# Kernel optimization log

Measured on AMD Instinct MI355X. Metric: run time of the kernel, lower is better.

Reference implementation:

```python
import jax, jax.numpy as jnp
import numpy as np

NSIDE_SEND, NSIDE_REC = 128, 64
NPIX_SEND = 12 * NSIDE_SEND * NSIDE_SEND  # 196608 edges (one per fine pixel)
NPIX_REC = 12 * NSIDE_REC * NSIDE_REC     # 49152 coarse pixels
RATIO = NPIX_SEND // NPIX_REC             # 4 children per coarse pixel
B, F_IN = 2, 128
EMBED_OUT, LIN_OUT = 64, 128
LIN_IN = EMBED_OUT + F_IN


def setup_inputs() -> dict:
    key = jax.random.key(0)
    ks = jax.random.split(key, 9)
    s = 0.02
    # buffers (deterministic, from HEALPix nested ordering)
    edge_attr = (jnp.arange(NPIX_SEND, dtype=jnp.float32) % RATIO).reshape(-1, 1)
    edge_rec = (jnp.arange(NPIX_SEND, dtype=jnp.int32) // RATIO)
    return {
        "x": jax.random.normal(ks[0], (B, NPIX_SEND, F_IN), dtype=jnp.float32),
        "edge_attr": edge_attr,
        "edge_rec": edge_rec,
        # edge embedder MLP: 1 -> 64 -> 64
        "we1": jax.random.normal(ks[1], (1, EMBED_OUT), dtype=jnp.float32) * s,
        "be1": jnp.zeros((EMBED_OUT,), dtype=jnp.float32),
        "we2": jax.random.normal(ks[2], (EMBED_OUT, EMBED_OUT), dtype=jnp.float32) * s,
        "be2": jnp.zeros((EMBED_OUT,), dtype=jnp.float32),
        # final FeedForward: 192 -> 128 -> 128
        "wf1": jax.random.normal(ks[3], (LIN_IN, LIN_OUT), dtype=jnp.float32) * s,
        "bf1": jnp.zeros((LIN_OUT,), dtype=jnp.float32),
        "wf2": jax.random.normal(ks[4], (LIN_OUT, LIN_OUT), dtype=jnp.float32) * s,
        "bf2": jnp.zeros((LIN_OUT,), dtype=jnp.float32),
    }


def reference(x, edge_attr, edge_rec, we1, be1, we2, be2, wf1, bf1, wf2, bf2):
    # edge embedding MLP over the per-edge scalar attribute  [E, embed_out]
    e = jax.nn.gelu(edge_attr @ we1 + be1) @ we2 + be2
    # broadcast over batch and concat with node features  [B, E, lin_in]
    vm = jnp.concatenate([jnp.broadcast_to(e[None], (x.shape[0],) + e.shape), x], axis=-1)
    # scatter_sum over receiver pixels along the edge axis  [B, R, lin_in]
    agg = jax.vmap(lambda v: jax.ops.segment_sum(v, edge_rec, num_segments=NPIX_REC))(vm)
    # final FeedForward
    return jax.nn.gelu(agg @ wf1 + bf1) @ wf2 + bf2
```

## Files before the change

kernel.cpp:

```cpp
#include <hip/hip_runtime.h>


#define NPIX_SEND 196608
#define NPIX_REC  49152
#define F_IN      128
#define EMB       64
#define LIN_OUT   128
#define MTOT      98304
#define BM        64
#define NBLOCKS   (MTOT / BM)

#define WS_C1 0
#define WS_W1 512
#define WS_W2 (512 + 32768)

#define LDS_H 0
#define LDS_W 16384
#define LDS_BYTES 49152

typedef __attribute__((ext_vector_type(4))) float f32x4;
typedef __attribute__((ext_vector_type(8))) short bf16x8;

__device__ __forceinline__ float gelu_tanh(float v) {
  float u = 0.7978845608028654f * (v + 0.044715f * v * v * v);
  float e = __expf(2.0f * u);
  return 0.5f * v * (1.0f + (1.0f - 2.0f / (e + 1.0f)));
}

__device__ __forceinline__ unsigned short f2bf(float f) {
  unsigned int u = __builtin_bit_cast(unsigned int, f);
  u += 0x7FFFu + ((u >> 16) & 1u);
  return (unsigned short)(u >> 16);
}

__global__ void heal_prep(const float* __restrict__ we1, const float* __restrict__ be1,
                          const float* __restrict__ we2, const float* __restrict__ be2,
                          const float* __restrict__ wf1, const float* __restrict__ bf1,
                          const float* __restrict__ wf2,
                          unsigned char* __restrict__ ws) {
  int t = threadIdx.x;
  if (blockIdx.x == 0) {
    __shared__ float G[EMB];
    __shared__ float esum[EMB];
    if (t < EMB) {
      float w = we1[t], b = be1[t];
      float g = 0.f;
      #pragma unroll
      for (int a = 0; a < 4; ++a) g += gelu_tanh((float)a * w + b);
      G[t] = g;
    }
    __syncthreads();
    if (t < EMB) {
      float s = 4.0f * be2[t];
      for (int h = 0; h < EMB; ++h) s += G[h] * we2[h * EMB + t];
      esum[t] = s;
    }
    __syncthreads();
    if (t < LIN_OUT) {
      float s = bf1[t];
      for (int i = 0; i < EMB; ++i) s += esum[i] * wf1[i * LIN_OUT + t];
      ((float*)(ws + WS_C1))[t] = s;
    }
  } else {
    int e0 = (blockIdx.x - 1) * 512 + t * 2;
    #pragma unroll
    for (int u = 0; u < 2; ++u) {
      int e = e0 + u;
      int idx = e & 16383;
      int n = idx >> 7;
      int k = idx & 127;
      float v;
      unsigned int base;
      if (e < 16384) { v = wf1[(EMB + k) * LIN_OUT + n]; base = WS_W1; }
      else           { v = wf2[k * LIN_OUT + n];         base = WS_W2; }
      unsigned int byte = (unsigned int)(n * 256 + k * 2) ^ (unsigned int)((n & 7) << 4);
      *(unsigned short*)(ws + base + byte) = f2bf(v);
    }
  }
}

__global__ __launch_bounds__(256, 3) void heal_main(
    const float* __restrict__ x, const float* __restrict__ bf2,
    const unsigned char* __restrict__ ws, float* __restrict__ out) {
  extern __shared__ unsigned char smem[];
  const int t = threadIdx.x;

  {
    const uint4* src = (const uint4*)(ws + WS_W1);
    uint4* dst = (uint4*)(smem + LDS_W);
    #pragma unroll
    for (int i = 0; i < 8; ++i) dst[t + 256 * i] = src[t + 256 * i];
  }
  uint4 w2reg[8];
  {
    const uint4* src2 = (const uint4*)(ws + WS_W2);
    #pragma unroll
    for (int i = 0; i < 8; ++i) w2reg[i] = src2[t + 256 * i];
  }

  const int gr0 = blockIdx.x * BM;
  const int b   = gr0 / NPIX_REC;
  const int rr0 = gr0 - b * NPIX_REC;
  const float* xb = x + (size_t)(b * NPIX_SEND + 4 * rr0) * F_IN;
  {
    const int kq = t & 31;
    const int mg = t >> 5;
    #pragma unroll
    for (int it = 0; it < 8; ++it) {
      int m = mg + it * 8;
      const f32x4* rp = (const f32x4*)(xb + (size_t)(4 * m) * F_IN) + kq;
      f32x4 s = rp[0] + rp[32] + rp[64] + rp[96];
      unsigned int lo = (unsigned int)f2bf(s.x) | ((unsigned int)f2bf(s.y) << 16);
      unsigned int hi = (unsigned int)f2bf(s.z) | ((unsigned int)f2bf(s.w) << 16);
      unsigned int byte = (unsigned int)(m * 256 + kq * 8) ^ (unsigned int)((m & 7) << 4);
      uint2 val; val.x = lo; val.y = hi;
      *(uint2*)(smem + LDS_H + byte) = val;
    }
  }

  const int w  = t >> 6;
  const int l  = t & 63;
  const int cr = l & 15;
  const int kg = l >> 4;
  float c1v[8], b2v[8];
  {
    const float* c1 = (const float*)(ws + WS_C1);
    #pragma unroll
    for (int f = 0; f < 8; ++f) { c1v[f] = c1[f * 16 + cr]; b2v[f] = bf2[f * 16 + cr]; }
  }

  __syncthreads();

  const int arow = w * 16 + cr;
  const unsigned int aswz = (unsigned int)((arow & 7) << 4);
  const unsigned int abase = (unsigned int)(arow * 256 + kg * 16);
  const unsigned int bswz = (unsigned int)((cr & 7) << 4);

  bf16x8 a[4];
  #pragma unroll
  for (int kk = 0; kk < 4; ++kk)
    a[kk] = *(const bf16x8*)(smem + LDS_H + ((abase + kk * 64) ^ aswz));

  f32x4 acc[8];
  #pragma unroll
  for (int f = 0; f < 8; ++f) {
    f32x4 z = {0.f, 0.f, 0.f, 0.f};
    acc[f] = z;
    unsigned int nbase = (unsigned int)((f * 16 + cr) * 256 + kg * 16);
    #pragma unroll
    for (int kk = 0; kk < 4; ++kk) {
      bf16x8 bfrag = *(const bf16x8*)(smem + LDS_W + ((nbase + kk * 64) ^ bswz));
      acc[f] = __builtin_amdgcn_mfma_f32_16x16x32_bf16(a[kk], bfrag, acc[f], 0, 0, 0);
    }
  }

  #pragma unroll
  for (int f = 0; f < 8; ++f) {
    #pragma unroll
    for (int q = 0; q < 4; ++q) {
      float v = gelu_tanh(acc[f][q] + c1v[f]);
      int hrow = w * 16 + kg * 4 + q;
      unsigned int byte = (unsigned int)(hrow * 256 + (f * 16 + cr) * 2)
                        ^ (unsigned int)((hrow & 7) << 4);
      *(unsigned short*)(smem + LDS_H + byte) = f2bf(v);
    }
  }

  __syncthreads();

  bf16x8 a2[4];
  #pragma unroll
  for (int kk = 0; kk < 4; ++kk)
    a2[kk] = *(const bf16x8*)(smem + LDS_H + ((abase + kk * 64) ^ aswz));

  {
    uint4* dst = (uint4*)(smem + LDS_W);
    #pragma unroll
    for (int i = 0; i < 8; ++i) dst[t + 256 * i] = w2reg[i];
  }
  __syncthreads();

  f32x4 acc2[8];
  #pragma unroll
  for (int f = 0; f < 8; ++f) {
    f32x4 z = {0.f, 0.f, 0.f, 0.f};
    acc2[f] = z;
    unsigned int nbase = (unsigned int)((f * 16 + cr) * 256 + kg * 16);
    #pragma unroll
    for (int kk = 0; kk < 4; ++kk) {
      bf16x8 bfrag = *(const bf16x8*)(smem + LDS_W + ((nbase + kk * 64) ^ bswz));
      acc2[f] = __builtin_amdgcn_mfma_f32_16x16x32_bf16(a2[kk], bfrag, acc2[f], 0, 0, 0);
    }
  }

  #pragma unroll
  for (int q = 0; q < 4; ++q) {
    int orow = gr0 + w * 16 + kg * 4 + q;
    float* op = out + (size_t)orow * LIN_OUT;
    #pragma unroll
    for (int f = 0; f < 8; ++f)
      op[f * 16 + cr] = acc2[f][q] + b2v[f];
  }
}

extern "C" void kernel_launch(void* const* d_in, const int* in_sizes, int n_in,
                              void* d_out, int out_size, void* d_ws, size_t ws_size,
                              hipStream_t stream) {
  const float* x   = (const float*)d_in[0];
  const float* we1 = (const float*)d_in[3];
  const float* be1 = (const float*)d_in[4];
  const float* we2 = (const float*)d_in[5];
  const float* be2 = (const float*)d_in[6];
  const float* wf1 = (const float*)d_in[7];
  const float* bf1 = (const float*)d_in[8];
  const float* wf2 = (const float*)d_in[9];
  const float* bf2 = (const float*)d_in[10];
  float* out = (float*)d_out;
  unsigned char* ws = (unsigned char*)d_ws;

  hipLaunchKernelGGL(heal_prep, dim3(65), dim3(256), 0, stream,
                     we1, be1, we2, be2, wf1, bf1, wf2, ws);
  hipLaunchKernelGGL(heal_main, dim3(NBLOCKS), dim3(256), LDS_BYTES, stream,
                     x, bf2, ws, out);
}
```

Measured before the change: 70.45 us.

## Stream weights in half-tiles through smaller LDS to raise occupancy

Splits each 128x128 weight matrix into two 64-column halves staged one at a time through a 16 KB LDS buffer, cutting LDS from 48 KB to 32 KB and register-held weights from 8 to 4 uint4 per thread, with launch bounds raised to 4 blocks per CU. Each wave now gathers its own 16 rows of x, and the x reads use nontemporal loads. The aim is more resident blocks to hide the memory-bound x reads. In exchange it adds several extra __syncthreads and LDS refills per block.

```diff
diff --git a/kernel.cpp b/kernel.cpp
--- a/kernel.cpp
+++ b/kernel.cpp
@@ -14,9 +14,9 @@
 #define WS_W1 512
 #define WS_W2 (512 + 32768)
 
-#define LDS_H 0
-#define LDS_W 16384
-#define LDS_BYTES 49152
+#define LDS_X 0
+#define LDS_B 16384
+#define LDS_BYTES 32768
 
 typedef __attribute__((ext_vector_type(4))) float f32x4;
 typedef __attribute__((ext_vector_type(8))) short bf16x8;
@@ -79,56 +79,49 @@
   }
 }
 
-__global__ __launch_bounds__(256, 3) void heal_main(
+__global__ __launch_bounds__(256, 4) void heal_main(
     const float* __restrict__ x, const float* __restrict__ bf2,
     const unsigned char* __restrict__ ws, float* __restrict__ out) {
   extern __shared__ unsigned char smem[];
   const int t = threadIdx.x;
-
-  {
-    const uint4* src = (const uint4*)(ws + WS_W1);
-    uint4* dst = (uint4*)(smem + LDS_W);
-    #pragma unroll
-    for (int i = 0; i < 8; ++i) dst[t + 256 * i] = src[t + 256 * i];
-  }
-  uint4 w2reg[8];
-  {
-    const uint4* src2 = (const uint4*)(ws + WS_W2);
-    #pragma unroll
-    for (int i = 0; i < 8; ++i) w2reg[i] = src2[t + 256 * i];
-  }
+  const int w = t >> 6, l = t & 63;
+  const int cr = l & 15, kg = l >> 4;
 
   const int gr0 = blockIdx.x * BM;
   const int b   = gr0 / NPIX_REC;
   const int rr0 = gr0 - b * NPIX_REC;
   const float* xb = x + (size_t)(b * NPIX_SEND + 4 * rr0) * F_IN;
-  {
-    const int kq = t & 31;
-    const int mg = t >> 5;
+
+  uint4 wregA[4], wregB[4];
+
+  {
+    const uint4* src = (const uint4*)(ws + WS_W1);
+    #pragma unroll
+    for (int i = 0; i < 4; ++i) wregA[i] = src[t + 256 * i];
+  }
+  {
+    const int kq = l & 31;
+    const int rh = l >> 5;
     #pragma unroll
     for (int it = 0; it < 8; ++it) {
-      int m = mg + it * 8;
+      int m = w * 16 + it * 2 + rh;
       const f32x4* rp = (const f32x4*)(xb + (size_t)(4 * m) * F_IN) + kq;
-      f32x4 s = rp[0] + rp[32] + rp[64] + rp[96];
+      f32x4 s = __builtin_nontemporal_load(rp)
+              + __builtin_nontemporal_load(rp + 32)
+              + __builtin_nontemporal_load(rp + 64)
+              + __builtin_nontemporal_load(rp + 96);
       unsigned int lo = (unsigned int)f2bf(s.x) | ((unsigned int)f2bf(s.y) << 16);
       unsigned int hi = (unsigned int)f2bf(s.z) | ((unsigned int)f2bf(s.w) << 16);
       unsigned int byte = (unsigned int)(m * 256 + kq * 8) ^ (unsigned int)((m & 7) << 4);
       uint2 val; val.x = lo; val.y = hi;
-      *(uint2*)(smem + LDS_H + byte) = val;
-    }
-  }
-
-  const int w  = t >> 6;
-  const int l  = t & 63;
-  const int cr = l & 15;
-  const int kg = l >> 4;
-  float c1v[8], b2v[8];
-  {
-    const float* c1 = (const float*)(ws + WS_C1);
-    #pragma unroll
-    for (int f = 0; f < 8; ++f) { c1v[f] = c1[f * 16 + cr]; b2v[f] = bf2[f * 16 + cr]; }
-  }
-
+      *(uint2*)(smem + LDS_X + byte) = val;
+    }
+  }
+  {
+    uint4* dst = (uint4*)(smem + LDS_B);
+    #pragma unroll
+    for (int i = 0; i < 4; ++i) dst[t + 256 * i] = wregA[i];
+  }
   __syncthreads();
 
   const int arow = w * 16 + cr;
@@ -139,67 +132,145 @@
   bf16x8 a[4];
   #pragma unroll
   for (int kk = 0; kk < 4; ++kk)
-    a[kk] = *(const bf16x8*)(smem + LDS_H + ((abase + kk * 64) ^ aswz));
-
-  f32x4 acc[8];
-  #pragma unroll
-  for (int f = 0; f < 8; ++f) {
-    f32x4 z = {0.f, 0.f, 0.f, 0.f};
-    acc[f] = z;
-    unsigned int nbase = (unsigned int)((f * 16 + cr) * 256 + kg * 16);
-    #pragma unroll
-    for (int kk = 0; kk < 4; ++kk) {
-      bf16x8 bfrag = *(const bf16x8*)(smem + LDS_W + ((nbase + kk * 64) ^ bswz));
-      acc[f] = __builtin_amdgcn_mfma_f32_16x16x32_bf16(a[kk], bfrag, acc[f], 0, 0, 0);
-    }
-  }
-
-  #pragma unroll
-  for (int f = 0; f < 8; ++f) {
+    a[kk] = *(const bf16x8*)(smem + LDS_X + ((abase + kk * 64) ^ aswz));
+  {
+    const uint4* src = (const uint4*)(ws + WS_W1 + 16384);
+    #pragma unroll
+    for (int i = 0; i < 4; ++i) wregB[i] = src[t + 256 * i];
+  }
+  f32x4 acc0[4], acc1[4];
+  #pragma unroll
+  for (int f = 0; f < 4; ++f) {
+    f32x4 z = {0.f, 0.f, 0.f, 0.f};
+    acc0[f] = z;
+    unsigned int nbase = (unsigned int)((f * 16 + cr) * 256 + kg * 16);
+    #pragma unroll
+    for (int kk = 0; kk < 4; ++kk) {
+      bf16x8 bfrag = *(const bf16x8*)(smem + LDS_B + ((nbase + kk * 64) ^ bswz));
+      acc0[f] = __builtin_amdgcn_mfma_f32_16x16x32_bf16(a[kk], bfrag, acc0[f], 0, 0, 0);
+    }
+  }
+  __syncthreads();
+
+  {
+    uint4* dst = (uint4*)(smem + LDS_B);
+    #pragma unroll
+    for (int i = 0; i < 4; ++i) dst[t + 256 * i] = wregB[i];
+  }
+  {
+    const uint4* src = (const uint4*)(ws + WS_W2);
+    #pragma unroll
+    for (int i = 0; i < 4; ++i) wregA[i] = src[t + 256 * i];
+  }
+  {
+    const float* c1 = (const float*)(ws + WS_C1);
+    #pragma unroll
+    for (int f = 0; f < 4; ++f) {
+      float c1v = c1[f * 16 + cr];
+      #pragma unroll
+      for (int q = 0; q < 4; ++q) {
+        float v = gelu_tanh(acc0[f][q] + c1v);
+        int hrow = w * 16 + kg * 4 + q;
+        unsigned int byte = (unsigned int)(hrow * 256 + (f * 16 + cr) * 2)
+                          ^ (unsigned int)((hrow & 7) << 4);
+        *(unsigned short*)(smem + LDS_X + byte) = f2bf(v);
+      }
+    }
+  }
+  __syncthreads();
+
+  #pragma unroll
+  for (int f = 0; f < 4; ++f) {
+    f32x4 z = {0.f, 0.f, 0.f, 0.f};
+    acc1[f] = z;
+    unsigned int nbase = (unsigned int)((f * 16 + cr) * 256 + kg * 16);
+    #pragma unroll
+    for (int kk = 0; kk < 4; ++kk) {
+      bf16x8 bfrag = *(const bf16x8*)(smem + LDS_B + ((nbase + kk * 64) ^ bswz));
+      acc1[f] = __builtin_amdgcn_mfma_f32_16x16x32_bf16(a[kk], bfrag, acc1[f], 0, 0, 0);
+    }
+  }
+  __syncthreads();
+
+  {
+    uint4* dst = (uint4*)(smem + LDS_B);
+    #pragma unroll
+    for (int i = 0; i < 4; ++i) dst[t + 256 * i] = wregA[i];
+  }
+  {
+    const uint4* src = (const uint4*)(ws + WS_W2 + 16384);
+    #pragma unroll
+    for (int i = 0; i < 4; ++i) wregB[i] = src[t + 256 * i];
+  }
+  {
+    const float* c1 = (const float*)(ws + WS_C1);
+    #pragma unroll
+    for (int f = 0; f < 4; ++f) {
+      float c1v = c1[64 + f * 16 + cr];
+      #pragma unroll
+      for (int q = 0; q < 4; ++q) {
+        float v = gelu_tanh(acc1[f][q] + c1v);
+        int hrow = w * 16 + kg * 4 + q;
+        unsigned int byte = (unsigned int)(hrow * 256 + (64 + f * 16 + cr) * 2)
+                          ^ (unsigned int)((hrow & 7) << 4);
+        *(unsigned short*)(smem + LDS_X + byte) = f2bf(v);
+      }
+    }
+  }
+  __syncthreads();
+
+  bf16x8 a2[4];
+  #pragma unroll
+  for (int kk = 0; kk < 4; ++kk)
+    a2[kk] = *(const bf16x8*)(smem + LDS_X + ((abase + kk * 64) ^ aswz));
+  #pragma unroll
+  for (int f = 0; f < 4; ++f) {
+    f32x4 z = {0.f, 0.f, 0.f, 0.f};
+    acc0[f] = z;
+    unsigned int nbase = (unsigned int)((f * 16 + cr) * 256 + kg * 16);
+    #pragma unroll
+    for (int kk = 0; kk < 4; ++kk) {
+      bf16x8 bfrag = *(const bf16x8*)(smem + LDS_B + ((nbase + kk * 64) ^ bswz));
+      acc0[f] = __builtin_amdgcn_mfma_f32_16x16x32_bf16(a2[kk], bfrag, acc0[f], 0, 0, 0);
+    }
+  }
+  #pragma unroll
+  for (int f = 0; f < 4; ++f) {
+    float b2 = bf2[f * 16 + cr];
     #pragma unroll
     for (int q = 0; q < 4; ++q) {
-      float v = gelu_tanh(acc[f][q] + c1v[f]);
-      int hrow = w * 16 + kg * 4 + q;
-      unsigned int byte = (unsigned int)(hrow * 256 + (f * 16 + cr) * 2)
-                        ^ (unsigned int)((hrow & 7) << 4);
-      *(unsigned short*)(smem + LDS_H + byte) = f2bf(v);
-    }
-  }
-
-  __syncthreads();
-
-  bf16x8 a2[4];
-  #pragma unroll
-  for (int kk = 0; kk < 4; ++kk)
-    a2[kk] = *(const bf16x8*)(smem + LDS_H + ((abase + kk * 64) ^ aswz));
-
-  {
-    uint4* dst = (uint4*)(smem + LDS_W);
-    #pragma unroll
-    for (int i = 0; i < 8; ++i) dst[t + 256 * i] = w2reg[i];
-  }
-  __syncthreads();
-
-  f32x4 acc2[8];
-  #pragma unroll
-  for (int f = 0; f < 8; ++f) {
-    f32x4 z = {0.f, 0.f, 0.f, 0.f};
-    acc2[f] = z;
-    unsigned int nbase = (unsigned int)((f * 16 + cr) * 256 + kg * 16);
-    #pragma unroll
-    for (int kk = 0; kk < 4; ++kk) {
-      bf16x8 bfrag = *(const bf16x8*)(smem + LDS_W + ((nbase + kk * 64) ^ bswz));
-      acc2[f] = __builtin_amdgcn_mfma_f32_16x16x32_bf16(a2[kk], bfrag, acc2[f], 0, 0, 0);
-    }
-  }
-
-  #pragma unroll
-  for (int q = 0; q < 4; ++q) {
-    int orow = gr0 + w * 16 + kg * 4 + q;
-    float* op = out + (size_t)orow * LIN_OUT;
-    #pragma unroll
-    for (int f = 0; f < 8; ++f)
-      op[f * 16 + cr] = acc2[f][q] + b2v[f];
+      int orow = gr0 + w * 16 + kg * 4 + q;
+      out[(size_t)orow * LIN_OUT + f * 16 + cr] = acc0[f][q] + b2;
+    }
+  }
+  __syncthreads();
+
+  {
+    uint4* dst = (uint4*)(smem + LDS_B);
+    #pragma unroll
+    for (int i = 0; i < 4; ++i) dst[t + 256 * i] = wregB[i];
+  }
+  __syncthreads();
+
+  #pragma unroll
+  for (int f = 0; f < 4; ++f) {
+    f32x4 z = {0.f, 0.f, 0.f, 0.f};
+    acc1[f] = z;
+    unsigned int nbase = (unsigned int)((f * 16 + cr) * 256 + kg * 16);
+    #pragma unroll
+    for (int kk = 0; kk < 4; ++kk) {
+      bf16x8 bfrag = *(const bf16x8*)(smem + LDS_B + ((nbase + kk * 64) ^ bswz));
+      acc1[f] = __builtin_amdgcn_mfma_f32_16x16x32_bf16(a2[kk], bfrag, acc1[f], 0, 0, 0);
+    }
+  }
+  #pragma unroll
+  for (int f = 0; f < 4; ++f) {
+    float b2 = bf2[64 + f * 16 + cr];
+    #pragma unroll
+    for (int q = 0; q < 4; ++q) {
+      int orow = gr0 + w * 16 + kg * 4 + q;
+      out[(size_t)orow * LIN_OUT + 64 + f * 16 + cr] = acc1[f][q] + b2;
+    }
   }
 }
 
```

New measurement: 85.09 us. +20.8%, slower.

## Read MFMA weight fragments from global/L2 and drop block barriers

Applied to the files above, without the earlier changes.

The weight matrices are no longer staged in LDS. Each wave now loads its B fragments directly from the workspace in global memory, which should stay hot in L2 and L1. This removes the per-block weight copy, the register-held W2, and all __syncthreads, because each wave only touches its own 16 rows of the hidden tile in LDS. LDS shrinks from 48KB to 16KB and launch bounds go from 3 to 4 blocks per CU. The cost is repeated global or cache loads of weights by every wave.

```diff
diff --git a/kernel.cpp b/kernel.cpp
--- a/kernel.cpp
+++ b/kernel.cpp
@@ -13,10 +13,6 @@
 #define WS_C1 0
 #define WS_W1 512
 #define WS_W2 (512 + 32768)
-
-#define LDS_H 0
-#define LDS_W 16384
-#define LDS_BYTES 49152
 
 typedef __attribute__((ext_vector_type(4))) float f32x4;
 typedef __attribute__((ext_vector_type(8))) short bf16x8;
@@ -73,133 +69,114 @@
       unsigned int base;
       if (e < 16384) { v = wf1[(EMB + k) * LIN_OUT + n]; base = WS_W1; }
       else           { v = wf2[k * LIN_OUT + n];         base = WS_W2; }
-      unsigned int byte = (unsigned int)(n * 256 + k * 2) ^ (unsigned int)((n & 7) << 4);
-      *(unsigned short*)(ws + base + byte) = f2bf(v);
-    }
-  }
-}
-
-__global__ __launch_bounds__(256, 3) void heal_main(
+      *(unsigned short*)(ws + base + (unsigned int)(n * 256 + k * 2)) = f2bf(v);
+    }
+  }
+}
+
+__global__ __launch_bounds__(256, 4) void heal_main(
     const float* __restrict__ x, const float* __restrict__ bf2,
     const unsigned char* __restrict__ ws, float* __restrict__ out) {
-  extern __shared__ unsigned char smem[];
+  __shared__ unsigned char smem[16384];
   const int t = threadIdx.x;
-
-  {
-    const uint4* src = (const uint4*)(ws + WS_W1);
-    uint4* dst = (uint4*)(smem + LDS_W);
-    #pragma unroll
-    for (int i = 0; i < 8; ++i) dst[t + 256 * i] = src[t + 256 * i];
-  }
-  uint4 w2reg[8];
-  {
-    const uint4* src2 = (const uint4*)(ws + WS_W2);
-    #pragma unroll
-    for (int i = 0; i < 8; ++i) w2reg[i] = src2[t + 256 * i];
-  }
+  const int w = t >> 6, l = t & 63;
+  const int cr = l & 15, kg = l >> 4;
 
   const int gr0 = blockIdx.x * BM;
   const int b   = gr0 / NPIX_REC;
   const int rr0 = gr0 - b * NPIX_REC;
   const float* xb = x + (size_t)(b * NPIX_SEND + 4 * rr0) * F_IN;
+
   {
-    const int kq = t & 31;
-    const int mg = t >> 5;
-    #pragma unroll
+    const int kq = l & 31;
+    const int rh = l >> 5;
+    #pragma unroll 2
     for (int it = 0; it < 8; ++it) {
-      int m = mg + it * 8;
+      int m = w * 16 + it * 2 + rh;
       const f32x4* rp = (const f32x4*)(xb + (size_t)(4 * m) * F_IN) + kq;
       f32x4 s = rp[0] + rp[32] + rp[64] + rp[96];
       unsigned int lo = (unsigned int)f2bf(s.x) | ((unsigned int)f2bf(s.y) << 16);
       unsigned int hi = (unsigned int)f2bf(s.z) | ((unsigned int)f2bf(s.w) << 16);
       unsigned int byte = (unsigned int)(m * 256 + kq * 8) ^ (unsigned int)((m & 7) << 4);
       uint2 val; val.x = lo; val.y = hi;
-      *(uint2*)(smem + LDS_H + byte) = val;
-    }
-  }
-
-  const int w  = t >> 6;
-  const int l  = t & 63;
-  const int cr = l & 15;
-  const int kg = l >> 4;
-  float c1v[8], b2v[8];
-  {
-    const float* c1 = (const float*)(ws + WS_C1);
-    #pragma unroll
-    for (int f = 0; f < 8; ++f) { c1v[f] = c1[f * 16 + cr]; b2v[f] = bf2[f * 16 + cr]; }
-  }
-
-  __syncthreads();
+      *(uint2*)(smem + byte) = val;
+    }
+  }
 
   const int arow = w * 16 + cr;
   const unsigned int aswz = (unsigned int)((arow & 7) << 4);
   const unsigned int abase = (unsigned int)(arow * 256 + kg * 16);
-  const unsigned int bswz = (unsigned int)((cr & 7) << 4);
 
   bf16x8 a[4];
   #pragma unroll
   for (int kk = 0; kk < 4; ++kk)
-    a[kk] = *(const bf16x8*)(smem + LDS_H + ((abase + kk * 64) ^ aswz));
-
-  f32x4 acc[8];
-  #pragma unroll
-  for (int f = 0; f < 8; ++f) {
-    f32x4 z = {0.f, 0.f, 0.f, 0.f};
-    acc[f] = z;
-    unsigned int nbase = (unsigned int)((f * 16 + cr) * 256 + kg * 16);
-    #pragma unroll
-    for (int kk = 0; kk < 4; ++kk) {
-      bf16x8 bfrag = *(const bf16x8*)(smem + LDS_W + ((nbase + kk * 64) ^ bswz));
-      acc[f] = __builtin_amdgcn_mfma_f32_16x16x32_bf16(a[kk], bfrag, acc[f], 0, 0, 0);
-    }
-  }
-
-  #pragma unroll
-  for (int f = 0; f < 8; ++f) {
+    a[kk] = *(const bf16x8*)(smem + ((abase + kk * 64) ^ aswz));
+
+  const float* c1 = (const float*)(ws + WS_C1);
+  const unsigned char* wg1 = ws + WS_W1;
+  const unsigned char* wg2 = ws + WS_W2;
+
+  #pragma unroll
+  for (int fp = 0; fp < 4; ++fp) {
+    const int f0 = fp * 2, f1 = f0 + 1;
+    const unsigned int n0 = (unsigned int)((f0 * 16 + cr) * 256 + kg * 16);
+    const unsigned int n1 = (unsigned int)((f1 * 16 + cr) * 256 + kg * 16);
+    bf16x8 b0[4], b1[4];
+    #pragma unroll
+    for (int kk = 0; kk < 4; ++kk) {
+      b0[kk] = *(const bf16x8*)(wg1 + n0 + kk * 64);
+      b1[kk] = *(const bf16x8*)(wg1 + n1 + kk * 64);
+    }
+    f32x4 acc0 = {0.f, 0.f, 0.f, 0.f}, acc1 = {0.f, 0.f, 0.f, 0.f};
+    #pragma unroll
+    for (int kk = 0; kk < 4; ++kk) {
+      acc0 = __builtin_amdgcn_mfma_f32_16x16x32_bf16(a[kk], b0[kk], acc0, 0, 0, 0);
+      acc1 = __builtin_amdgcn_mfma_f32_16x16x32_bf16(a[kk], b1[kk], acc1, 0, 0, 0);
+    }
+    float c10 = c1[f0 * 16 + cr], c11 = c1[f1 * 16 + cr];
     #pragma unroll
     for (int q = 0; q < 4; ++q) {
-      float v = gelu_tanh(acc[f][q] + c1v[f]);
       int hrow = w * 16 + kg * 4 + q;
-      unsigned int byte = (unsigned int)(hrow * 256 + (f * 16 + cr) * 2)
-                        ^ (unsigned int)((hrow & 7) << 4);
-      *(unsigned short*)(smem + LDS_H + byte) = f2bf(v);
-    }
-  }
-
-  __syncthreads();
+      unsigned int hswz = (unsigned int)((hrow & 7) << 4);
+      float v0 = gelu_tanh(acc0[q] + c10);
+      float v1 = gelu_tanh(acc1[q] + c11);
+      unsigned int byte0 = ((unsigned int)(hrow * 256 + (f0 * 16 + cr) * 2)) ^ hswz;
+      unsigned int byte1 = ((unsigned int)(hrow * 256 + (f1 * 16 + cr) * 2)) ^ hswz;
+      *(unsigned short*)(smem + byte0) = f2bf(v0);
+      *(unsigned short*)(smem + byte1) = f2bf(v1);
+    }
+  }
 
   bf16x8 a2[4];
   #pragma unroll
   for (int kk = 0; kk < 4; ++kk)
-    a2[kk] = *(const bf16x8*)(smem + LDS_H + ((abase + kk * 64) ^ aswz));
-
-  {
-    uint4* dst = (uint4*)(smem + LDS_W);
-    #pragma unroll
-    for (int i = 0; i < 8; ++i) dst[t + 256 * i] = w2reg[i];
-  }
-  __syncthreads();
-
-  f32x4 acc2[8];
-  #pragma unroll
-  for (int f = 0; f < 8; ++f) {
-    f32x4 z = {0.f, 0.f, 0.f, 0.f};
-    acc2[f] = z;
-    unsigned int nbase = (unsigned int)((f * 16 + cr) * 256 + kg * 16);
-    #pragma unroll
-    for (int kk = 0; kk < 4; ++kk) {
-      bf16x8 bfrag = *(const bf16x8*)(smem + LDS_W + ((nbase + kk * 64) ^ bswz));
-      acc2[f] = __builtin_amdgcn_mfma_f32_16x16x32_bf16(a2[kk], bfrag, acc2[f], 0, 0, 0);
-    }
-  }
-
-  #pragma unroll
-  for (int q = 0; q < 4; ++q) {
-    int orow = gr0 + w * 16 + kg * 4 + q;
-    float* op = out + (size_t)orow * LIN_OUT;
-    #pragma unroll
-    for (int f = 0; f < 8; ++f)
-      op[f * 16 + cr] = acc2[f][q] + b2v[f];
+    a2[kk] = *(const bf16x8*)(smem + ((abase + kk * 64) ^ aswz));
+
+  #pragma unroll
+  for (int fp = 0; fp < 4; ++fp) {
+    const int f0 = fp * 2, f1 = f0 + 1;
+    const unsigned int n0 = (unsigned int)((f0 * 16 + cr) * 256 + kg * 16);
+    const unsigned int n1 = (unsigned int)((f1 * 16 + cr) * 256 + kg * 16);
+    bf16x8 b0[4], b1[4];
+    #pragma unroll
+    for (int kk = 0; kk < 4; ++kk) {
+      b0[kk] = *(const bf16x8*)(wg2 + n0 + kk * 64);
+      b1[kk] = *(const bf16x8*)(wg2 + n1 + kk * 64);
+    }
+    f32x4 acc0 = {0.f, 0.f, 0.f, 0.f}, acc1 = {0.f, 0.f, 0.f, 0.f};
+    #pragma unroll
+    for (int kk = 0; kk < 4; ++kk) {
+      acc0 = __builtin_amdgcn_mfma_f32_16x16x32_bf16(a2[kk], b0[kk], acc0, 0, 0, 0);
+      acc1 = __builtin_amdgcn_mfma_f32_16x16x32_bf16(a2[kk], b1[kk], acc1, 0, 0, 0);
+    }
+    float b20 = bf2[f0 * 16 + cr], b21 = bf2[f1 * 16 + cr];
+    #pragma unroll
+    for (int q = 0; q < 4; ++q) {
+      int orow = gr0 + w * 16 + kg * 4 + q;
+      float* op = out + (size_t)orow * LIN_OUT;
+      op[f0 * 16 + cr] = acc0[q] + b20;
+      op[f1 * 16 + cr] = acc1[q] + b21;
+    }
   }
 }
 
@@ -220,6 +197,6 @@
 
   hipLaunchKernelGGL(heal_prep, dim3(65), dim3(256), 0, stream,
                      we1, be1, we2, be2, wf1, bf1, wf2, ws);
-  hipLaunchKernelGGL(heal_main, dim3(NBLOCKS), dim3(256), LDS_BYTES, stream,
+  hipLaunchKernelGGL(heal_main, dim3(NBLOCKS), dim3(256), 0, stream,
                      x, bf2, ws, out);
 }
```

Measured after the change: 74.83 us. +6.2%, slower.

## Split child-pixel summation into a separate kernel writing bf16 aggregates

Applied to the files above, without the earlier changes.

Moves the 4-way child summation of x and the bf16 conversion out of the main GEMM kernel into a dedicated streaming kernel that writes a compact bf16 buffer to workspace. The main kernel then loads pre-aggregated bf16 rows into LDS instead of reading fp32 x. The aim is to decouple the bandwidth-bound reduction from the MFMA kernel, which runs with limited occupancy. The cost is an extra launch plus writing and re-reading an intermediate buffer of about 25 MB.

```diff
diff --git a/kernel.cpp b/kernel.cpp
--- a/kernel.cpp
+++ b/kernel.cpp
@@ -13,8 +13,9 @@
 #define WS_C1 0
 #define WS_W1 512
 #define WS_W2 (512 + 32768)
-
-#define LDS_H 0
+#define WS_XS 131072
+
+#define LDS_X 0
 #define LDS_W 16384
 #define LDS_BYTES 49152
 
@@ -79,8 +80,27 @@
   }
 }
 
+__global__ void heal_xsum(const float* __restrict__ x, unsigned int* __restrict__ xs) {
+  size_t j = (size_t)blockIdx.x * 256 + threadIdx.x;
+  size_t m = j >> 4;
+  int c = (int)(j & 15);
+  const f32x4* p = (const f32x4*)(x + (m * 4) * F_IN) + c * 2;
+  f32x4 a0 = p[0],  a1 = p[1];
+  f32x4 b0 = p[32], b1 = p[33];
+  f32x4 c0 = p[64], c1 = p[65];
+  f32x4 d0 = p[96], d1 = p[97];
+  f32x4 s0 = (a0 + b0) + (c0 + d0);
+  f32x4 s1 = (a1 + b1) + (c1 + d1);
+  uint4 o;
+  o.x = (unsigned int)f2bf(s0.x) | ((unsigned int)f2bf(s0.y) << 16);
+  o.y = (unsigned int)f2bf(s0.z) | ((unsigned int)f2bf(s0.w) << 16);
+  o.z = (unsigned int)f2bf(s1.x) | ((unsigned int)f2bf(s1.y) << 16);
+  o.w = (unsigned int)f2bf(s1.z) | ((unsigned int)f2bf(s1.w) << 16);
+  *(uint4*)(xs + j * 4) = o;
+}
+
 __global__ __launch_bounds__(256, 3) void heal_main(
-    const float* __restrict__ x, const float* __restrict__ bf2,
+    const unsigned char* __restrict__ xs, const float* __restrict__ bf2,
     const unsigned char* __restrict__ ws, float* __restrict__ out) {
   extern __shared__ unsigned char smem[];
   const int t = threadIdx.x;
@@ -99,22 +119,16 @@
   }
 
   const int gr0 = blockIdx.x * BM;
-  const int b   = gr0 / NPIX_REC;
-  const int rr0 = gr0 - b * NPIX_REC;
-  const float* xb = x + (size_t)(b * NPIX_SEND + 4 * rr0) * F_IN;
-  {
-    const int kq = t & 31;
-    const int mg = t >> 5;
-    #pragma unroll
-    for (int it = 0; it < 8; ++it) {
-      int m = mg + it * 8;
-      const f32x4* rp = (const f32x4*)(xb + (size_t)(4 * m) * F_IN) + kq;
-      f32x4 s = rp[0] + rp[32] + rp[64] + rp[96];
-      unsigned int lo = (unsigned int)f2bf(s.x) | ((unsigned int)f2bf(s.y) << 16);
-      unsigned int hi = (unsigned int)f2bf(s.z) | ((unsigned int)f2bf(s.w) << 16);
-      unsigned int byte = (unsigned int)(m * 256 + kq * 8) ^ (unsigned int)((m & 7) << 4);
-      uint2 val; val.x = lo; val.y = hi;
-      *(uint2*)(smem + LDS_H + byte) = val;
+  {
+    const int kq2 = t & 15;
+    const int r0  = t >> 4;
+    const uint4* src = (const uint4*)(xs + (size_t)gr0 * 256);
+    #pragma unroll
+    for (int it = 0; it < 4; ++it) {
+      int r = r0 + it * 16;
+      uint4 v = src[r * 16 + kq2];
+      unsigned int byte = (unsigned int)(r * 256 + kq2 * 16) ^ (unsigned int)((r & 7) << 4);
+      *(uint4*)(smem + LDS_X + byte) = v;
     }
   }
 
@@ -139,7 +153,7 @@
   bf16x8 a[4];
   #pragma unroll
   for (int kk = 0; kk < 4; ++kk)
-    a[kk] = *(const bf16x8*)(smem + LDS_H + ((abase + kk * 64) ^ aswz));
+    a[kk] = *(const bf16x8*)(smem + LDS_X + ((abase + kk * 64) ^ aswz));
 
   f32x4 acc[8];
   #pragma unroll
@@ -162,7 +176,7 @@
       int hrow = w * 16 + kg * 4 + q;
       unsigned int byte = (unsigned int)(hrow * 256 + (f * 16 + cr) * 2)
                         ^ (unsigned int)((hrow & 7) << 4);
-      *(unsigned short*)(smem + LDS_H + byte) = f2bf(v);
+      *(unsigned short*)(smem + LDS_X + byte) = f2bf(v);
     }
   }
 
@@ -171,7 +185,7 @@
   bf16x8 a2[4];
   #pragma unroll
   for (int kk = 0; kk < 4; ++kk)
-    a2[kk] = *(const bf16x8*)(smem + LDS_H + ((abase + kk * 64) ^ aswz));
+    a2[kk] = *(const bf16x8*)(smem + LDS_X + ((abase + kk * 64) ^ aswz));
 
   {
     uint4* dst = (uint4*)(smem + LDS_W);
@@ -220,6 +234,8 @@
 
   hipLaunchKernelGGL(heal_prep, dim3(65), dim3(256), 0, stream,
                      we1, be1, we2, be2, wf1, bf1, wf2, ws);
+  hipLaunchKernelGGL(heal_xsum, dim3(6144), dim3(256), 0, stream,
+                     x, (unsigned int*)(ws + WS_XS));
   hipLaunchKernelGGL(heal_main, dim3(NBLOCKS), dim3(256), LDS_BYTES, stream,
-                     x, bf2, ws, out);
-}
+                     (const unsigned char*)(ws + WS_XS), bf2, ws, out);
+}
```

Result: slower. 74.66 us (+6.0%).
